# Optimization experiments

Measured on AMD Instinct MI355X. Metric: run time of the kernel, lower is better.

## Reference

```python
import jax, jax.numpy as jnp
import numpy as np
from jax import lax

NEG = -9.0e15
ALPHA = 0.2  # LeakyReLU slope

def _cnn(x, conv1_w, conv1_b, conv2_w, conv2_b):
    # x: (BN,1,9,9)
    dn = ('NCHW', 'OIHW', 'NCHW')
    y = lax.conv_general_dilated(x, conv1_w, (1, 1), 'SAME', dimension_numbers=dn)
    y = jax.nn.relu(y + conv1_b[None, :, None, None])
    y = lax.conv_general_dilated(y, conv2_w, (1, 1), 'VALID', dimension_numbers=dn)
    y = jax.nn.relu(y + conv2_b[None, :, None, None])
    return y.reshape(y.shape[0], -1)  # (BN, 32*7*7=1568)

def _gat(h, adj, W, a1, a2):
    # h: (B,N,F) ; adj: (B,N,N) int
    Wh = h @ W                                  # (B,N,D)
    # a([Wh_i ; Wh_j]) == Wh_i@a1 + Wh_j@a2  (exact split of the concat linear)
    s1 = Wh @ a1                                # (B,N) query-node term
    s2 = Wh @ a2                                # (B,N) key-node term
    e = jax.nn.leaky_relu(s1[:, :, None] + s2[:, None, :], ALPHA)  # (B,N,N)
    e = jnp.where(adj > 0, e, NEG)
    attn = jax.nn.softmax(e, axis=-1)           # dropout off (eval mode)
    h_prime = jnp.einsum('bij,bjd->bid', attn, Wh)
    return jax.nn.elu(h_prime)

def reference(obs_grids, adj_matrix, conv1_w, conv1_b, conv2_w, conv2_b,
              W, a1, a2, actor_w, actor_b, critic_w, critic_b):
    B, N, C, H, Wd = obs_grids.shape
    feats = _cnn(obs_grids.reshape(B * N, C, H, Wd), conv1_w, conv1_b, conv2_w, conv2_b)
    feats = feats.reshape(B, N, -1)             # (B,N,1568)
    emb = _gat(feats, adj_matrix, W, a1, a2)    # (B,N,64)
    logits = emb @ actor_w + actor_b            # (B,N,n_actions)
    values = emb @ critic_w + critic_b          # (B,N,1)
    return (logits, values)

def setup_inputs() -> dict:
    key = jax.random.key(0)
    ks = jax.random.split(key, 12)
    B, N, H, Wd = 8, 1024, 9, 9
    FEAT, HID, NA = 1568, 64, 16
    f32 = jnp.float32
    inp = {}
    inp['obs_grids'] = jax.random.normal(ks[0], (B, N, 1, H, Wd), f32)
    inp['adj_matrix'] = jax.random.randint(ks[1], (B, N, N), 0, 2, jnp.int32)
    inp['conv1_w'] = jax.random.normal(ks[2], (16, 1, 3, 3), f32) * 0.1
    inp['conv1_b'] = jnp.zeros((16,), f32)
    inp['conv2_w'] = jax.random.normal(ks[3], (32, 16, 3, 3), f32) * 0.05
    inp['conv2_b'] = jnp.zeros((32,), f32)
    inp['W'] = jax.random.normal(ks[4], (FEAT, HID), f32) * (1.0 / np.sqrt(FEAT))
    inp['a1'] = jax.random.normal(ks[5], (HID,), f32) * 0.1
    inp['a2'] = jax.random.normal(ks[6], (HID,), f32) * 0.1
    inp['actor_w'] = jax.random.normal(ks[7], (HID, NA), f32) * (1.0 / np.sqrt(HID))
    inp['actor_b'] = jnp.zeros((NA,), f32)
    inp['critic_w'] = jax.random.normal(ks[8], (HID, 1), f32) * (1.0 / np.sqrt(HID))
    inp['critic_b'] = jnp.zeros((1,), f32)
    return inp
```

## Files before the change

### kernel.cpp

```cpp
#include <hip/hip_runtime.h>
#include <math.h>

#define NEG_BIG (-9.0e15f)

typedef __attribute__((ext_vector_type(8))) short short8;
typedef __attribute__((ext_vector_type(4))) short short4v;
typedef __attribute__((ext_vector_type(4))) float f32x4;

__device__ __forceinline__ short f32_to_bf16_bits(float f) {
  union { float f; unsigned u; } cv; cv.f = f;
  unsigned r = (cv.u + 0x7fffu + ((cv.u >> 16) & 1u)) >> 16;
  return (short)r;
}

#define KPAD 1664
__global__ __launch_bounds__(256) void wt_prep(const float* __restrict__ W,
                                               short* __restrict__ Wt) {
  int idx = blockIdx.x * 256 + threadIdx.x;
  if (idx < 64 * KPAD) {
    int n = idx / KPAD, kk = idx - n * KPAD;
    int o = kk / 52, p = kk - o * 52;
    float v = (p < 49) ? W[(o * 49 + p) * 64 + n] : 0.0f;
    Wt[idx] = f32_to_bf16_bits(v);
  }
}

#define IPB 8
#define FSTR 1672
__global__ __launch_bounds__(256, 4) void cnn_gemm_kernel(
    const float* __restrict__ obs, const float* __restrict__ w1,
    const float* __restrict__ b1, const float* __restrict__ w2,
    const float* __restrict__ b2, const short* __restrict__ Wt,
    const float* __restrict__ a1, const float* __restrict__ a2,
    short* __restrict__ Whb, float* __restrict__ s1, float* __restrict__ s2)
{
  __shared__ __align__(16) float sw1p[192];
  __shared__ float sb2[32];
  __shared__ __align__(16) short wt[32 * 144];
  __shared__ float sinp[IPB * 121];
  __shared__ __align__(16) short ubuf[IPB * FSTR];
  int tid = threadIdx.x;
  long inst0 = (long)blockIdx.x * IPB;

  for (int i = tid; i < 192; i += 256) {
    int c = i / 12, k = i - c * 12;
    float v = (k < 9) ? w1[c * 9 + k] : ((k == 9) ? b1[c] : 0.0f);
    sw1p[i] = v;
  }
  if (tid < 32) sb2[tid] = b2[tid];
  {
    int o = tid >> 3, kp0 = tid & 7;
    #pragma unroll
    for (int m = 0; m < 18; ++m) {
      int kp = kp0 + m * 8;
      int kstep = kp >> 5, which = (kp >> 4) & 1, ci = kp & 15;
      int tap = kstep * 2 + which;
      wt[o * 144 + kp] = f32_to_bf16_bits(w2[o * 144 + ci * 9 + tap]);
    }
  }
  for (int i = tid; i < IPB * 121; i += 256) {
    int inst = i / 121, rem = i - inst * 121;
    int py = rem / 11, px = rem - py * 11;
    float v = 0.f;
    if (py >= 1 && py <= 9 && px >= 1 && px <= 9)
      v = obs[(inst0 + inst) * 81 + (py - 1) * 9 + (px - 1)];
    sinp[inst * 121 + rem] = v;
  }
  for (int i = tid; i < IPB * 188; i += 256) {
    int inst = i / 188, q = i - inst * 188;
    *(unsigned*)&ubuf[inst * FSTR + 1296 + q * 2] = 0u;
  }
  __syncthreads();

  {
    int inst = tid >> 5, s = tid & 31;
    const float* ib = &sinp[inst * 121];
    short* hw = &ubuf[inst * FSTR];
    float inr[3][9];
    #pragma unroll
    for (int t = 0; t < 3; ++t) {
      int px = s + t * 32;
      if (px < 81) {
        int y = (px * 456) >> 12;
        const float* ip = ib + px + 2 * y;
        inr[t][0] = ip[0];  inr[t][1] = ip[1];  inr[t][2] = ip[2];
        inr[t][3] = ip[11]; inr[t][4] = ip[12]; inr[t][5] = ip[13];
        inr[t][6] = ip[22]; inr[t][7] = ip[23]; inr[t][8] = ip[24];
      }
    }
    #pragma unroll
    for (int cp = 0; cp < 8; ++cp) {
      int c0 = cp * 2, c1 = cp * 2 + 1;
      float4 wa0 = *(const float4*)&sw1p[c0 * 12];
      float4 wb0 = *(const float4*)&sw1p[c0 * 12 + 4];
      float4 wc0 = *(const float4*)&sw1p[c0 * 12 + 8];
      float4 wa1 = *(const float4*)&sw1p[c1 * 12];
      float4 wb1 = *(const float4*)&sw1p[c1 * 12 + 4];
      float4 wc1 = *(const float4*)&sw1p[c1 * 12 + 8];
      #pragma unroll
      for (int t = 0; t < 3; ++t) {
        int px = s + t * 32;
        if (px < 81) {
          float v0 = wc0.y
            + inr[t][0] * wa0.x + inr[t][1] * wa0.y + inr[t][2] * wa0.z
            + inr[t][3] * wa0.w + inr[t][4] * wb0.x + inr[t][5] * wb0.y
            + inr[t][6] * wb0.z + inr[t][7] * wb0.w + inr[t][8] * wc0.x;
          float v1 = wc1.y
            + inr[t][0] * wa1.x + inr[t][1] * wa1.y + inr[t][2] * wa1.z
            + inr[t][3] * wa1.w + inr[t][4] * wb1.x + inr[t][5] * wb1.y
            + inr[t][6] * wb1.z + inr[t][7] * wb1.w + inr[t][8] * wc1.x;
          v0 = fmaxf(v0, 0.f); v1 = fmaxf(v1, 0.f);
          unsigned pk = (unsigned)(unsigned short)f32_to_bf16_bits(v0)
                      | ((unsigned)(unsigned short)f32_to_bf16_bits(v1) << 16);
          int idx = (px * 16 + c0) ^ (((px >> 2) & 3) << 3);
          *(unsigned*)&hw[idx] = pk;
        }
      }
    }
  }

  int lane = tid & 63;
  int wv = tid >> 6;
  int g = lane >> 4;
  int which = g >> 1;
  int half = g & 1;
  int colr = lane & 15;

  const int offtab[9] = {0, 1, 2, 9, 10, 11, 18, 19, 20};
  int myoff[5];
  #pragma unroll
  for (int k = 0; k < 5; ++k) {
    int tap = k * 2 + which;
    myoff[k] = (tap < 9) ? offtab[tap] : 0;
  }
  int posm[4];
  #pragma unroll
  for (int mt = 0; mt < 4; ++mt) {
    int p = mt * 16 + colr;
    posm[mt] = (p < 49) ? (p / 7) * 9 + (p % 7) : 0;
  }
  short8 bfw[2][5];
  #pragma unroll
  for (int nt = 0; nt < 2; ++nt) {
    #pragma unroll
    for (int k = 0; k < 4; ++k)
      bfw[nt][k] = *(const short8*)&wt[(nt * 16 + colr) * 144 + k * 32 + g * 8];
    if (which == 0) {
      bfw[nt][4] = *(const short8*)&wt[(nt * 16 + colr) * 144 + 128 + half * 8];
    } else {
      short8 z = {0, 0, 0, 0, 0, 0, 0, 0};
      bfw[nt][4] = z;
    }
  }

  #pragma unroll
  for (int ii = 0; ii < 2; ++ii) {
    int inst = wv * 2 + ii;
    const short* hb = &ubuf[inst * FSTR];
    short* fb = &ubuf[inst * FSTR];
    f32x4 acc[4][2];
    #pragma unroll
    for (int mt = 0; mt < 4; ++mt) {
      short8 af[5];
      #pragma unroll
      for (int k = 0; k < 5; ++k) {
        int row = posm[mt] + myoff[k];
        int idx = (row * 16 + half * 8) ^ (((row >> 2) & 3) << 3);
        af[k] = *(const short8*)&hb[idx];
      }
      #pragma unroll
      for (int nt = 0; nt < 2; ++nt) {
        f32x4 a0 = {0.f, 0.f, 0.f, 0.f};
        #pragma unroll
        for (int k = 0; k < 5; ++k)
          a0 = __builtin_amdgcn_mfma_f32_16x16x32_bf16(af[k], bfw[nt][k], a0, 0, 0, 0);
        acc[mt][nt] = a0;
      }
    }
    #pragma unroll
    for (int mt = 0; mt < 3; ++mt) {
      #pragma unroll
      for (int nt = 0; nt < 2; ++nt) {
        int o = nt * 16 + colr;
        float bias = sb2[o];
        short4v pk;
        #pragma unroll
        for (int r = 0; r < 4; ++r)
          pk[r] = f32_to_bf16_bits(fmaxf(acc[mt][nt][r] + bias, 0.f));
        *(short4v*)&fb[o * 52 + mt * 16 + g * 4] = pk;
      }
    }
    if (g == 0) {
      #pragma unroll
      for (int nt = 0; nt < 2; ++nt) {
        int o = nt * 16 + colr;
        fb[o * 52 + 48] = f32_to_bf16_bits(fmaxf(acc[3][nt][0] + sb2[o], 0.f));
      }
    }
  }
  __syncthreads();

  {
    int arow = colr & 7;
    const short* Wrow = Wt + (wv * 16 + colr) * KPAD;
    f32x4 acc_e = {0.f, 0.f, 0.f, 0.f};
    f32x4 acc_o = {0.f, 0.f, 0.f, 0.f};
    for (int ks = 0; ks < 52; ks += 2) {
      short8 af0 = *(const short8*)&ubuf[arow * FSTR + ks * 32 + g * 8];
      short8 bf0 = *(const short8*)&Wrow[ks * 32 + g * 8];
      short8 af1 = *(const short8*)&ubuf[arow * FSTR + (ks + 1) * 32 + g * 8];
      short8 bf1 = *(const short8*)&Wrow[(ks + 1) * 32 + g * 8];
      acc_e = __builtin_amdgcn_mfma_f32_16x16x32_bf16(af0, bf0, acc_e, 0, 0, 0);
      acc_o = __builtin_amdgcn_mfma_f32_16x16x32_bf16(af1, bf1, acc_o, 0, 0, 0);
    }
    f32x4 acc2;
    #pragma unroll
    for (int r = 0; r < 4; ++r) acc2[r] = acc_e[r] + acc_o[r];
    float a1c = a1[wv * 16 + colr];
    float a2c = a2[wv * 16 + colr];
    float* sp1 = sinp;
    float* sp2 = sinp + 32;
    if (g < 2) {
      long bidx = inst0 >> 10;
      int node0 = (int)(inst0 & 1023) + g * 4;
      short4v pk;
      #pragma unroll
      for (int r = 0; r < 4; ++r) pk[r] = f32_to_bf16_bits(acc2[r]);
      *(short4v*)&Whb[(bidx * 64 + wv * 16 + colr) * 1024 + node0] = pk;
      #pragma unroll
      for (int r = 0; r < 4; ++r) {
        int inst = g * 4 + r;
        float v = acc2[r];
        float x1 = v * a1c, x2 = v * a2c;
        #pragma unroll
        for (int w = 1; w < 16; w <<= 1) { x1 += __shfl_xor(x1, w); x2 += __shfl_xor(x2, w); }
        if (colr == 0) { sp1[wv * 8 + inst] = x1; sp2[wv * 8 + inst] = x2; }
      }
    }
  }
  __syncthreads();
  if (tid < 8) {
    float* sp1 = sinp;
    float* sp2 = sinp + 32;
    s1[inst0 + tid] = sp1[tid] + sp1[8 + tid] + sp1[16 + tid] + sp1[24 + tid];
    s2[inst0 + tid] = sp2[tid] + sp2[8 + tid] + sp2[16 + tid] + sp2[24 + tid];
  }
}

#define PSTR2 1096
__global__ __launch_bounds__(256) void gat_kernel(
    const int* __restrict__ adj, const short* __restrict__ Whb,
    const float* __restrict__ s1, const float* __restrict__ s2,
    const float* __restrict__ actor_w, const float* __restrict__ actor_b,
    const float* __restrict__ critic_w, const float* __restrict__ critic_b,
    float* __restrict__ out)
{
  __shared__ __align__(16) short pb[16 * PSTR2];
  __shared__ __align__(16) float s2s[1024];
  __shared__ float saw[64 * 16];
  __shared__ float scw[64];
  __shared__ float sab[16];
  __shared__ float denom[16];
  __shared__ float emb[16][65];
  int tid = threadIdx.x;
  int b = blockIdx.y;
  int i0 = blockIdx.x * 16;

  for (int j = tid; j < 1024; j += 256) s2s[j] = s2[b * 1024 + j];
  for (int idx2 = tid; idx2 < 64 * 16; idx2 += 256) saw[idx2] = actor_w[idx2];
  if (tid < 64) scw[tid] = critic_w[tid];
  if (tid < 16) sab[tid] = actor_b[tid];
  __syncthreads();

  {
    int il = tid >> 4, r = tid & 15;
    int i = i0 + il;
    float s1i = s1[b * 1024 + i];
    const int* arow = adj + ((long)(b * 1024 + i)) * 1024;
    unsigned long long amask = 0ull;
    float m = -3.0e38f;
    #pragma unroll
    for (int jj = 0; jj < 16; ++jj) {
      int j0 = jj * 64 + r * 4;
      int4 a4 = *(const int4*)&arow[j0];
      float4 sv = *(const float4*)&s2s[j0];
      float e0 = s1i + sv.x; e0 = (e0 > 0.f) ? e0 : 0.2f * e0;
      float e1 = s1i + sv.y; e1 = (e1 > 0.f) ? e1 : 0.2f * e1;
      float e2 = s1i + sv.z; e2 = (e2 > 0.f) ? e2 : 0.2f * e2;
      float e3 = s1i + sv.w; e3 = (e3 > 0.f) ? e3 : 0.2f * e3;
      if (a4.x > 0) { m = fmaxf(m, e0); amask |= 1ull << (jj * 4 + 0); }
      if (a4.y > 0) { m = fmaxf(m, e1); amask |= 1ull << (jj * 4 + 1); }
      if (a4.z > 0) { m = fmaxf(m, e2); amask |= 1ull << (jj * 4 + 2); }
      if (a4.w > 0) { m = fmaxf(m, e3); amask |= 1ull << (jj * 4 + 3); }
    }
    #pragma unroll
    for (int w = 1; w < 16; w <<= 1) m = fmaxf(m, __shfl_xor(m, w));
    float sum = 0.f;
    short* prow = &pb[il * PSTR2];
    #pragma unroll
    for (int jj = 0; jj < 16; ++jj) {
      int j0 = jj * 64 + r * 4;
      float4 sv = *(const float4*)&s2s[j0];
      float e0 = s1i + sv.x; e0 = (e0 > 0.f) ? e0 : 0.2f * e0;
      float e1 = s1i + sv.y; e1 = (e1 > 0.f) ? e1 : 0.2f * e1;
      float e2 = s1i + sv.z; e2 = (e2 > 0.f) ? e2 : 0.2f * e2;
      float e3 = s1i + sv.w; e3 = (e3 > 0.f) ? e3 : 0.2f * e3;
      float p0 = ((amask >> (jj * 4 + 0)) & 1ull) ? __expf(e0 - m) : 0.f;
      float p1 = ((amask >> (jj * 4 + 1)) & 1ull) ? __expf(e1 - m) : 0.f;
      float p2 = ((amask >> (jj * 4 + 2)) & 1ull) ? __expf(e2 - m) : 0.f;
      float p3 = ((amask >> (jj * 4 + 3)) & 1ull) ? __expf(e3 - m) : 0.f;
      sum += (p0 + p1) + (p2 + p3);
      short4v st;
      st[0] = f32_to_bf16_bits(p0); st[1] = f32_to_bf16_bits(p1);
      st[2] = f32_to_bf16_bits(p2); st[3] = f32_to_bf16_bits(p3);
      *(short4v*)&prow[j0] = st;
    }
    #pragma unroll
    for (int w = 1; w < 16; w <<= 1) sum += __shfl_xor(sum, w);
    if (r == 0) denom[il] = sum;
  }
  __syncthreads();

  {
    int lane = tid & 63, wv = tid >> 6, g = lane >> 4, colr = lane & 15;
    const short* Wcol = Whb + ((long)b * 64 + wv * 16 + colr) * 1024;
    const short* prow = &pb[colr * PSTR2];
    f32x4 acc = {0.f, 0.f, 0.f, 0.f};
    #pragma unroll
    for (int ks = 0; ks < 32; ++ks) {
      short8 af = *(const short8*)&prow[ks * 32 + g * 8];
      short8 bf = *(const short8*)&Wcol[ks * 32 + g * 8];
      acc = __builtin_amdgcn_mfma_f32_16x16x32_bf16(af, bf, acc, 0, 0, 0);
    }
    #pragma unroll
    for (int rr = 0; rr < 4; ++rr) {
      int row = g * 4 + rr;
      float v = acc[rr] / denom[row];
      v = (v > 0.f) ? v : expm1f(v);
      emb[row][wv * 16 + colr] = v;
    }
  }
  __syncthreads();

  {
    int il = tid >> 4, na = tid & 15;
    float accl = sab[na];
    #pragma unroll
    for (int d = 0; d < 64; ++d) accl += emb[il][d] * saw[d * 16 + na];
    out[((long)(b * 1024 + i0 + il)) * 16 + na] = accl;
  }
  if (tid < 16) {
    float v = critic_b[0];
    #pragma unroll
    for (int d = 0; d < 64; ++d) v += emb[tid][d] * scw[d];
    out[131072 + b * 1024 + i0 + tid] = v;
  }
}

extern "C" void kernel_launch(void* const* d_in, const int* in_sizes, int n_in,
                              void* d_out, int out_size, void* d_ws, size_t ws_size,
                              hipStream_t stream)
{
  const float* obs = (const float*)d_in[0];
  const int*   adj = (const int*)d_in[1];
  const float* c1w = (const float*)d_in[2];
  const float* c1b = (const float*)d_in[3];
  const float* c2w = (const float*)d_in[4];
  const float* c2b = (const float*)d_in[5];
  const float* W   = (const float*)d_in[6];
  const float* a1  = (const float*)d_in[7];
  const float* a2  = (const float*)d_in[8];
  const float* aw  = (const float*)d_in[9];
  const float* ab  = (const float*)d_in[10];
  const float* cw  = (const float*)d_in[11];
  const float* cb  = (const float*)d_in[12];
  float* out = (float*)d_out;
  float* ws = (float*)d_ws;

  short* Whb = (short*)ws;
  float* s1  = ws + 262144;
  float* s2  = s1 + 8192;
  short* Wt  = (short*)(s2 + 8192);

  hipLaunchKernelGGL(wt_prep, dim3((64 * KPAD + 255) / 256), dim3(256), 0, stream, W, Wt);
  hipLaunchKernelGGL(cnn_gemm_kernel, dim3(1024), dim3(256), 0, stream,
                     obs, c1w, c1b, c2w, c2b, Wt, a1, a2, Whb, s1, s2);
  hipLaunchKernelGGL(gat_kernel, dim3(64, 8), dim3(256), 0, stream,
                     adj, Whb, s1, s2, aw, ab, cw, cb, out);
}
```

Before: 69.52 us.

## Halve GAT rows per block and prefetch W tiles before barrier in CNN GEMM

The GAT kernel now handles 8 query rows per block instead of 16, doubling the grid to 1024 blocks so more blocks stream the adjacency matrix concurrently. Each row is processed by 32 threads, and the MFMA duplicates rows to fill its 16-row tile. In the CNN kernel, the first four W fragments are loaded before the barrier and the K loop uses four independent accumulators to hide MFMA latency. In exchange, half the MFMA work in the GAT kernel is wasted and the Whb loads per output row double.

New measurement: 71.42 us. 1.03x slower.

```diff
diff --git a/kernel.cpp b/kernel.cpp
--- a/kernel.cpp
+++ b/kernel.cpp
@@ -198,24 +198,43 @@
       }
     }
   }
+
+  const short* Wrow = Wt + (wv * 16 + colr) * KPAD;
+  short8 pre0 = *(const short8*)&Wrow[0 * 32 + g * 8];
+  short8 pre1 = *(const short8*)&Wrow[1 * 32 + g * 8];
+  short8 pre2 = *(const short8*)&Wrow[2 * 32 + g * 8];
+  short8 pre3 = *(const short8*)&Wrow[3 * 32 + g * 8];
   __syncthreads();
 
   {
     int arow = colr & 7;
-    const short* Wrow = Wt + (wv * 16 + colr) * KPAD;
-    f32x4 acc_e = {0.f, 0.f, 0.f, 0.f};
-    f32x4 acc_o = {0.f, 0.f, 0.f, 0.f};
-    for (int ks = 0; ks < 52; ks += 2) {
-      short8 af0 = *(const short8*)&ubuf[arow * FSTR + ks * 32 + g * 8];
-      short8 bf0 = *(const short8*)&Wrow[ks * 32 + g * 8];
-      short8 af1 = *(const short8*)&ubuf[arow * FSTR + (ks + 1) * 32 + g * 8];
+    const short* Ab = &ubuf[arow * FSTR + g * 8];
+    f32x4 ac0, ac1, ac2, ac3;
+    ac0 = __builtin_amdgcn_mfma_f32_16x16x32_bf16(
+        *(const short8*)&Ab[0 * 32], pre0, (f32x4){0.f, 0.f, 0.f, 0.f}, 0, 0, 0);
+    ac1 = __builtin_amdgcn_mfma_f32_16x16x32_bf16(
+        *(const short8*)&Ab[1 * 32], pre1, (f32x4){0.f, 0.f, 0.f, 0.f}, 0, 0, 0);
+    ac2 = __builtin_amdgcn_mfma_f32_16x16x32_bf16(
+        *(const short8*)&Ab[2 * 32], pre2, (f32x4){0.f, 0.f, 0.f, 0.f}, 0, 0, 0);
+    ac3 = __builtin_amdgcn_mfma_f32_16x16x32_bf16(
+        *(const short8*)&Ab[3 * 32], pre3, (f32x4){0.f, 0.f, 0.f, 0.f}, 0, 0, 0);
+    for (int ks = 4; ks < 52; ks += 4) {
+      short8 af0 = *(const short8*)&Ab[(ks + 0) * 32];
+      short8 bf0 = *(const short8*)&Wrow[(ks + 0) * 32 + g * 8];
+      short8 af1 = *(const short8*)&Ab[(ks + 1) * 32];
       short8 bf1 = *(const short8*)&Wrow[(ks + 1) * 32 + g * 8];
-      acc_e = __builtin_amdgcn_mfma_f32_16x16x32_bf16(af0, bf0, acc_e, 0, 0, 0);
-      acc_o = __builtin_amdgcn_mfma_f32_16x16x32_bf16(af1, bf1, acc_o, 0, 0, 0);
+      short8 af2 = *(const short8*)&Ab[(ks + 2) * 32];
+      short8 bf2 = *(const short8*)&Wrow[(ks + 2) * 32 + g * 8];
+      short8 af3 = *(const short8*)&Ab[(ks + 3) * 32];
+      short8 bf3 = *(const short8*)&Wrow[(ks + 3) * 32 + g * 8];
+      ac0 = __builtin_amdgcn_mfma_f32_16x16x32_bf16(af0, bf0, ac0, 0, 0, 0);
+      ac1 = __builtin_amdgcn_mfma_f32_16x16x32_bf16(af1, bf1, ac1, 0, 0, 0);
+      ac2 = __builtin_amdgcn_mfma_f32_16x16x32_bf16(af2, bf2, ac2, 0, 0, 0);
+      ac3 = __builtin_amdgcn_mfma_f32_16x16x32_bf16(af3, bf3, ac3, 0, 0, 0);
     }
     f32x4 acc2;
     #pragma unroll
-    for (int r = 0; r < 4; ++r) acc2[r] = acc_e[r] + acc_o[r];
+    for (int r = 0; r < 4; ++r) acc2[r] = (ac0[r] + ac1[r]) + (ac2[r] + ac3[r]);
     float a1c = a1[wv * 16 + colr];
     float a2c = a2[wv * 16 + colr];
     float* sp1 = sinp;
@@ -247,6 +266,7 @@
   }
 }
 
+#define QR 8
 #define PSTR2 1096
 __global__ __launch_bounds__(256) void gat_kernel(
     const int* __restrict__ adj, const short* __restrict__ Whb,
@@ -255,16 +275,16 @@
     const float* __restrict__ critic_w, const float* __restrict__ critic_b,
     float* __restrict__ out)
 {
-  __shared__ __align__(16) short pb[16 * PSTR2];
+  __shared__ __align__(16) short pb[QR * PSTR2];
   __shared__ __align__(16) float s2s[1024];
   __shared__ float saw[64 * 16];
   __shared__ float scw[64];
   __shared__ float sab[16];
-  __shared__ float denom[16];
-  __shared__ float emb[16][65];
+  __shared__ float denom[QR];
+  __shared__ float emb[QR][65];
   int tid = threadIdx.x;
   int b = blockIdx.y;
-  int i0 = blockIdx.x * 16;
+  int i0 = blockIdx.x * QR;
 
   for (int j = tid; j < 1024; j += 256) s2s[j] = s2[b * 1024 + j];
   for (int idx2 = tid; idx2 < 64 * 16; idx2 += 256) saw[idx2] = actor_w[idx2];
@@ -273,42 +293,42 @@
   __syncthreads();
 
   {
-    int il = tid >> 4, r = tid & 15;
+    int il = tid >> 5, r = tid & 31;
     int i = i0 + il;
     float s1i = s1[b * 1024 + i];
     const int* arow = adj + ((long)(b * 1024 + i)) * 1024;
-    unsigned long long amask = 0ull;
+    unsigned amask = 0u;
     float m = -3.0e38f;
     #pragma unroll
-    for (int jj = 0; jj < 16; ++jj) {
-      int j0 = jj * 64 + r * 4;
+    for (int jj = 0; jj < 8; ++jj) {
+      int j0 = jj * 128 + r * 4;
       int4 a4 = *(const int4*)&arow[j0];
       float4 sv = *(const float4*)&s2s[j0];
       float e0 = s1i + sv.x; e0 = (e0 > 0.f) ? e0 : 0.2f * e0;
       float e1 = s1i + sv.y; e1 = (e1 > 0.f) ? e1 : 0.2f * e1;
       float e2 = s1i + sv.z; e2 = (e2 > 0.f) ? e2 : 0.2f * e2;
       float e3 = s1i + sv.w; e3 = (e3 > 0.f) ? e3 : 0.2f * e3;
-      if (a4.x > 0) { m = fmaxf(m, e0); amask |= 1ull << (jj * 4 + 0); }
-      if (a4.y > 0) { m = fmaxf(m, e1); amask |= 1ull << (jj * 4 + 1); }
-      if (a4.z > 0) { m = fmaxf(m, e2); amask |= 1ull << (jj * 4 + 2); }
-      if (a4.w > 0) { m = fmaxf(m, e3); amask |= 1ull << (jj * 4 + 3); }
-    }
-    #pragma unroll
-    for (int w = 1; w < 16; w <<= 1) m = fmaxf(m, __shfl_xor(m, w));
+      if (a4.x > 0) { m = fmaxf(m, e0); amask |= 1u << (jj * 4 + 0); }
+      if (a4.y > 0) { m = fmaxf(m, e1); amask |= 1u << (jj * 4 + 1); }
+      if (a4.z > 0) { m = fmaxf(m, e2); amask |= 1u << (jj * 4 + 2); }
+      if (a4.w > 0) { m = fmaxf(m, e3); amask |= 1u << (jj * 4 + 3); }
+    }
+    #pragma unroll
+    for (int w = 1; w < 32; w <<= 1) m = fmaxf(m, __shfl_xor(m, w));
     float sum = 0.f;
     short* prow = &pb[il * PSTR2];
     #pragma unroll
-    for (int jj = 0; jj < 16; ++jj) {
-      int j0 = jj * 64 + r * 4;
+    for (int jj = 0; jj < 8; ++jj) {
+      int j0 = jj * 128 + r * 4;
       float4 sv = *(const float4*)&s2s[j0];
       float e0 = s1i + sv.x; e0 = (e0 > 0.f) ? e0 : 0.2f * e0;
       float e1 = s1i + sv.y; e1 = (e1 > 0.f) ? e1 : 0.2f * e1;
       float e2 = s1i + sv.z; e2 = (e2 > 0.f) ? e2 : 0.2f * e2;
       float e3 = s1i + sv.w; e3 = (e3 > 0.f) ? e3 : 0.2f * e3;
-      float p0 = ((amask >> (jj * 4 + 0)) & 1ull) ? __expf(e0 - m) : 0.f;
-      float p1 = ((amask >> (jj * 4 + 1)) & 1ull) ? __expf(e1 - m) : 0.f;
-      float p2 = ((amask >> (jj * 4 + 2)) & 1ull) ? __expf(e2 - m) : 0.f;
-      float p3 = ((amask >> (jj * 4 + 3)) & 1ull) ? __expf(e3 - m) : 0.f;
+      float p0 = ((amask >> (jj * 4 + 0)) & 1u) ? __expf(e0 - m) : 0.f;
+      float p1 = ((amask >> (jj * 4 + 1)) & 1u) ? __expf(e1 - m) : 0.f;
+      float p2 = ((amask >> (jj * 4 + 2)) & 1u) ? __expf(e2 - m) : 0.f;
+      float p3 = ((amask >> (jj * 4 + 3)) & 1u) ? __expf(e3 - m) : 0.f;
       sum += (p0 + p1) + (p2 + p3);
       short4v st;
       st[0] = f32_to_bf16_bits(p0); st[1] = f32_to_bf16_bits(p1);
@@ -316,7 +336,7 @@
       *(short4v*)&prow[j0] = st;
     }
     #pragma unroll
-    for (int w = 1; w < 16; w <<= 1) sum += __shfl_xor(sum, w);
+    for (int w = 1; w < 32; w <<= 1) sum += __shfl_xor(sum, w);
     if (r == 0) denom[il] = sum;
   }
   __syncthreads();
@@ -324,7 +344,7 @@
   {
     int lane = tid & 63, wv = tid >> 6, g = lane >> 4, colr = lane & 15;
     const short* Wcol = Whb + ((long)b * 64 + wv * 16 + colr) * 1024;
-    const short* prow = &pb[colr * PSTR2];
+    const short* prow = &pb[(colr & 7) * PSTR2];
     f32x4 acc = {0.f, 0.f, 0.f, 0.f};
     #pragma unroll
     for (int ks = 0; ks < 32; ++ks) {
@@ -332,24 +352,26 @@
       short8 bf = *(const short8*)&Wcol[ks * 32 + g * 8];
       acc = __builtin_amdgcn_mfma_f32_16x16x32_bf16(af, bf, acc, 0, 0, 0);
     }
-    #pragma unroll
-    for (int rr = 0; rr < 4; ++rr) {
-      int row = g * 4 + rr;
-      float v = acc[rr] / denom[row];
-      v = (v > 0.f) ? v : expm1f(v);
-      emb[row][wv * 16 + colr] = v;
-    }
-  }
-  __syncthreads();
-
-  {
+    if (g < 2) {
+      #pragma unroll
+      for (int rr = 0; rr < 4; ++rr) {
+        int row = g * 4 + rr;
+        float v = acc[rr] / denom[row];
+        v = (v > 0.f) ? v : expm1f(v);
+        emb[row][wv * 16 + colr] = v;
+      }
+    }
+  }
+  __syncthreads();
+
+  if (tid < QR * 16) {
     int il = tid >> 4, na = tid & 15;
     float accl = sab[na];
     #pragma unroll
     for (int d = 0; d < 64; ++d) accl += emb[il][d] * saw[d * 16 + na];
     out[((long)(b * 1024 + i0 + il)) * 16 + na] = accl;
   }
-  if (tid < 16) {
+  if (tid < QR) {
     float v = critic_b[0];
     #pragma unroll
     for (int d = 0; d < 64; ++d) v += emb[tid][d] * scw[d];
@@ -385,6 +407,6 @@
   hipLaunchKernelGGL(wt_prep, dim3((64 * KPAD + 255) / 256), dim3(256), 0, stream, W, Wt);
   hipLaunchKernelGGL(cnn_gemm_kernel, dim3(1024), dim3(256), 0, stream,
                      obs, c1w, c1b, c2w, c2b, Wt, a1, a2, Whb, s1, s2);
-  hipLaunchKernelGGL(gat_kernel, dim3(64, 8), dim3(256), 0, stream,
+  hipLaunchKernelGGL(gat_kernel, dim3(128, 8), dim3(256), 0, stream,
                      adj, Whb, s1, s2, aw, ab, cw, cb, out);
 }
```
